# Kernel tuning notes

Measured on AMD Instinct MI355X. Metric: run time of the kernel, lower is better.

The kernel has to match this reference:

```python
import math
import jax
import jax.numpy as jnp
import numpy as np
from jax import lax

HEADS = 4
TOPK = 8


def _gelu(x):
    return jax.nn.gelu(x, approximate=False)


def _ln(x, g, b, eps=1e-5):
    m = x.mean(-1, keepdims=True)
    v = ((x - m) ** 2).mean(-1, keepdims=True)
    return (x - m) * lax.rsqrt(v + eps) * g + b


def setup_inputs() -> dict:
    key = jax.random.key(0)
    ks = jax.random.split(key, 16)
    B, T, N, C, A = 16, 16, 196, 768, 192

    def w(k, shape, s=0.02):
        return jax.random.normal(k, shape, jnp.float32) * s

    return dict(
        x=w(ks[0], (B, T, N + 1, C), 1.0),
        down_w=w(ks[1], (A, C)), down_b=jnp.zeros((A,), jnp.float32),
        ldw_w=w(ks[2], (A, 1, 3, 3), 0.1),
        lpw_w=w(ks[3], (A, A), 0.05),
        lnorm_g=jnp.ones((A,), jnp.float32), lnorm_b=jnp.zeros((A,), jnp.float32),
        tdw_w=w(ks[4], (A, 1, 3), 0.1),
        tpw_w=w(ks[5], (A, A), 0.05),
        tmlp_w1=w(ks[6], (2 * A, A), 0.05), tmlp_b1=jnp.zeros((2 * A,), jnp.float32),
        tmlp_w2=w(ks[7], (A, 2 * A), 0.05), tmlp_b2=jnp.zeros((A,), jnp.float32),
        tnorm_g=jnp.ones((A,), jnp.float32), tnorm_b=jnp.zeros((A,), jnp.float32),
        attn_in_w=w(ks[8], (3 * A, A), 0.05), attn_in_b=jnp.zeros((3 * A,), jnp.float32),
        attn_out_w=w(ks[9], (A, A), 0.05), attn_out_b=jnp.zeros((A,), jnp.float32),
        aproj_w=w(ks[10], (A, A), 0.05), aproj_b=jnp.zeros((A,), jnp.float32),
        anorm_g=jnp.ones((A,), jnp.float32), anorm_b=jnp.zeros((A,), jnp.float32),
        gate_w1=w(ks[11], (A, 2 * A), 0.05), gate_b1=jnp.zeros((A,), jnp.float32),
        gate_w2=w(ks[12], (3 * A, A), 0.05), gate_b2=jnp.zeros((3 * A,), jnp.float32),
        up_w=w(ks[13], (C, A), 0.02), up_b=jnp.zeros((C,), jnp.float32),
        cls_w=w(ks[14], (C, A), 0.02), cls_b=jnp.zeros((C,), jnp.float32),
    )


def reference(x, down_w, down_b, ldw_w, lpw_w, lnorm_g, lnorm_b, tdw_w, tpw_w,
              tmlp_w1, tmlp_b1, tmlp_w2, tmlp_b2, tnorm_g, tnorm_b,
              attn_in_w, attn_in_b, attn_out_w, attn_out_b, aproj_w, aproj_b,
              anorm_g, anorm_b, gate_w1, gate_b1, gate_w2, gate_b2,
              up_w, up_b, cls_w, cls_b):
    cls_tok = x[:, :, :1, :]
    patch = x[:, :, 1:, :]
    b, t, n, _ = patch.shape
    hw = int(math.isqrt(n))
    a = down_w.shape[0]

    # down projection: [b,t,n,C] -> [b,t,n,A]
    ph = jnp.einsum('btnc,ac->btna', patch, down_w) + down_b
    # temporal difference, delta[:,0]=0
    delta = jnp.concatenate([jnp.zeros_like(ph[:, :1]), ph[:, 1:] - ph[:, :-1]], axis=1)

    # --- local path: depthwise 3x3 -> GELU -> pointwise 1x1 -> LN ---
    loc = ph.reshape(b * t, hw, hw, a).transpose(0, 3, 1, 2)  # (bt) a h w
    loc = lax.conv_general_dilated(loc, ldw_w, (1, 1), 'SAME',
                                   feature_group_count=a,
                                   dimension_numbers=('NCHW', 'OIHW', 'NCHW'))
    loc = _gelu(loc)
    loc = jnp.einsum('bchw,dc->bdhw', loc, lpw_w)
    loc = loc.transpose(0, 2, 3, 1).reshape(b, t, n, a)
    local = _ln(loc, lnorm_g, lnorm_b)

    # --- transition path: depthwise temporal conv -> GELU -> pointwise -> MLP -> LN ---
    tr = delta.transpose(0, 2, 3, 1).reshape(b * n, a, t)  # (bn) a t
    tr = lax.conv_general_dilated(tr, tdw_w, (1,), 'SAME',
                                  feature_group_count=a,
                                  dimension_numbers=('NCH', 'OIH', 'NCH'))
    tr = _gelu(tr)
    tr = jnp.einsum('nct,dc->ndt', tr, tpw_w)
    tr = tr.reshape(b, n, a, t).transpose(0, 3, 1, 2)  # b t n a
    h1 = _gelu(jnp.einsum('btna,ha->btnh', tr, tmlp_w1) + tmlp_b1)
    tr = jnp.einsum('btnh,ah->btna', h1, tmlp_w2) + tmlp_b2
    transition = _ln(tr, tnorm_g, tnorm_b)

    # --- relation anchor path: topk gather -> temporal MHA -> scatter_add -> LN ---
    kk = min(TOPK, n)
    sal = jnp.abs(delta).mean(-1)  # b t n
    _, idx = lax.top_k(sal, kk)    # b t k
    bi = jnp.arange(b)[:, None, None]
    ti = jnp.arange(t)[None, :, None]
    anchor = (ph + delta)[bi, ti, idx]  # b t k a
    tok = anchor.transpose(0, 2, 1, 3).reshape(b * kk, t, a)  # (bk) t a
    qkv = tok @ attn_in_w.T + attn_in_b
    q, k_, v = jnp.split(qkv, 3, axis=-1)
    dh = a // HEADS

    def heads(z):
        return z.reshape(b * kk, t, HEADS, dh).transpose(0, 2, 1, 3)

    q, k_, v = heads(q), heads(k_), heads(v)
    att = jax.nn.softmax(jnp.einsum('bhqd,bhkd->bhqk', q, k_) / math.sqrt(dh), axis=-1)
    out = jnp.einsum('bhqk,bhkd->bhqd', att, v).transpose(0, 2, 1, 3).reshape(b * kk, t, a)
    out = out @ attn_out_w.T + attn_out_b
    out = out @ aproj_w.T + aproj_b
    anchor_tok = out.reshape(b, kk, t, a).transpose(0, 2, 1, 3)  # b t k a
    anchor_map = jnp.zeros_like(ph).at[bi, ti, idx].add(anchor_tok)
    anchor_map = _ln(anchor_map, anorm_g, anorm_b)

    # --- softmax-gated 3-way fusion ---
    dp = jnp.abs(delta).mean((1, 2))      # b a
    ap = anchor_tok.mean((1, 2))          # b a
    g = jnp.concatenate([dp, ap], axis=-1)
    g = _gelu(g @ gate_w1.T + gate_b1) @ gate_w2.T + gate_b2
    gw = jax.nn.softmax(g.reshape(b, 3, a), axis=1)[:, :, None, None, :]
    fused = gw[:, 0] * local + gw[:, 1] * transition + gw[:, 2] * anchor_map

    patch_out = patch + fused @ up_w.T + up_b
    cls_out = cls_tok + fused.mean(2, keepdims=True) @ cls_w.T + cls_b
    return jnp.concatenate([cls_out, patch_out], axis=2)
```

## Files before the change

### kernel.cpp

```cpp
#include <hip/hip_runtime.h>
#include <hip/hip_bf16.h>
#include <math.h>

constexpr int Bb  = 16;
constexpr int Tt  = 16;
constexpr int Nn  = 196;
constexpr int Cc  = 768;
constexpr int Aa  = 192;
constexpr int KK  = 8;
constexpr int NCAND = 16;
constexpr int BT  = Bb * Tt;
constexpr int BTN = BT * Nn;
constexpr int BKT = Bb * KK * Tt;
constexpr size_t SZ = (size_t)BTN * Aa;

typedef unsigned short ushortt;
typedef __attribute__((ext_vector_type(8))) short bf16x8;
typedef __attribute__((ext_vector_type(4))) float f32x4;
typedef __attribute__((ext_vector_type(4))) unsigned short u16x4;
typedef __attribute__((ext_vector_type(8))) unsigned short u16x8;

static __device__ __forceinline__ float gelu_f(float x) {
  return 0.5f * x * (1.0f + erff(x * 0.7071067811865476f));
}
static __device__ __forceinline__ ushortt f2bf(float f) {
  __hip_bfloat16 h = __float2bfloat16(f);
  return *reinterpret_cast<ushortt*>(&h);
}
static __device__ __forceinline__ float bf2f(ushortt u) {
  return __uint_as_float(((unsigned)u) << 16);
}
static __device__ __forceinline__ void gload16(const void* g, void* l) {
  __builtin_amdgcn_global_load_lds(
      (const __attribute__((address_space(1))) void*)g,
      (__attribute__((address_space(3))) void*)l, 16, 0, 0);
}

constexpr int S_down   = Aa * Cc;
constexpr int S_attnin = 3 * Aa * Aa;
constexpr int S_sq     = Aa * Aa;
constexpr int S_t      = 2 * Aa * Aa;
constexpr int O1 = S_down;
constexpr int O2 = O1 + S_attnin;
constexpr int O3 = O2 + S_sq;
constexpr int O4 = O3 + S_sq;
constexpr int O5 = O4 + S_sq;
constexpr int O6 = O5 + S_sq;
constexpr int O7 = O6 + S_t;
constexpr int O8 = O7 + S_t;
constexpr int OTOT = O8 + S_down;

__global__ void cvtw_kernel(const float* __restrict__ w0,
                            const float* __restrict__ w1,
                            const float* __restrict__ w2,
                            const float* __restrict__ w3,
                            const float* __restrict__ w4,
                            const float* __restrict__ w5,
                            const float* __restrict__ w6,
                            const float* __restrict__ w7,
                            const float* __restrict__ w8,
                            ushortt* __restrict__ outw) {
  int e = blockIdx.x * 256 + threadIdx.x;
  const float* src;
  int off;
  if (e < O1)      { src = w0; off = 0;  }
  else if (e < O2) { src = w1; off = O1; }
  else if (e < O3) { src = w2; off = O2; }
  else if (e < O4) { src = w3; off = O3; }
  else if (e < O5) { src = w4; off = O4; }
  else if (e < O6) { src = w5; off = O5; }
  else if (e < O7) { src = w6; off = O6; }
  else if (e < O8) { src = w7; off = O7; }
  else             { src = w8; off = O8; }
  outw[e] = f2bf(src[e - off]);
}

template <typename CT, int BIAS, int EPI>
__global__ __launch_bounds__(256) void gemm_lds(
    const ushortt* __restrict__ Ain, const ushortt* __restrict__ Wb,
    const float* __restrict__ bias, CT* __restrict__ Cout,
    const float* __restrict__ resid, int M, int Nc, int K) {
  __shared__ __align__(16) unsigned char smem[40960];
  ushortt (*As)[64 * 64] = (ushortt(*)[64 * 64])smem;
  ushortt (*Bs)[96 * 64] = (ushortt(*)[96 * 64])(smem + 2 * 64 * 64 * 2);
  const int tid = threadIdx.x;

  const int ncb = gridDim.x;
  const int nwg = ncb * gridDim.y;
  const int bid = blockIdx.y * ncb + blockIdx.x;
  const int cpx = nwg >> 3;
  const int swz = (bid & 7) * cpx + (bid >> 3);
  const int row0 = (swz / ncb) * 64;
  const int col0 = (swz % ncb) * 96;

  const int wid = tid >> 6;
  const int lane = tid & 63;
  const int wr = wid >> 1;
  const int wc = wid & 1;
  const int l15 = lane & 15;
  const int kgrp = lane >> 4;

  const int lr = lane >> 3;
  const int lc = 8 * ((lane & 7) ^ lr);

  f32x4 acc[2][3];
#pragma unroll
  for (int i = 0; i < 2; ++i)
#pragma unroll
    for (int j = 0; j < 3; ++j) acc[i][j] = (f32x4){0.f, 0.f, 0.f, 0.f};

#define ISSUE(buf, k0)                                                       \
  do {                                                                       \
    _Pragma("unroll") for (int i = 0; i < 2; ++i) {                          \
      int j = 2 * wid + i;                                                   \
      const ushortt* g =                                                     \
          Ain + (size_t)(row0 + 8 * j + lr) * K + (k0) + lc;                 \
      gload16(g, &As[buf][j * 512]);                                         \
    }                                                                        \
    _Pragma("unroll") for (int i = 0; i < 3; ++i) {                          \
      int j = 3 * wid + i;                                                   \
      const ushortt* g =                                                     \
          Wb + (size_t)(col0 + 8 * j + lr) * K + (k0) + lc;                  \
      gload16(g, &Bs[buf][j * 512]);                                         \
    }                                                                        \
  } while (0)

  ISSUE(0, 0);
  __syncthreads();

  const int nsteps = K >> 6;
  int cur = 0;
  for (int step = 0; step < nsteps; ++step) {
    const bool pref = (step + 1 < nsteps);
    if (pref) ISSUE(cur ^ 1, (step + 1) << 6);
#pragma unroll
    for (int kk = 0; kk < 2; ++kk) {
      const int cb = kk * 64 + kgrp * 16;
      bf16x8 af[2], bfv[3];
#pragma unroll
      for (int fm = 0; fm < 2; ++fm) {
        int r = wr * 32 + fm * 16 + l15;
        af[fm] = *(const bf16x8*)&As[cur][r * 64 +
                                          ((cb ^ ((r & 7) << 4)) >> 1)];
      }
#pragma unroll
      for (int fn = 0; fn < 3; ++fn) {
        int r = wc * 48 + fn * 16 + l15;
        bfv[fn] = *(const bf16x8*)&Bs[cur][r * 64 +
                                           ((cb ^ ((r & 7) << 4)) >> 1)];
      }
#pragma unroll
      for (int fm = 0; fm < 2; ++fm)
#pragma unroll
        for (int fn = 0; fn < 3; ++fn)
          acc[fm][fn] = __builtin_amdgcn_mfma_f32_16x16x32_bf16(
              af[fm], bfv[fn], acc[fm][fn], 0, 0, 0);
    }
    __syncthreads();
    cur ^= 1;
  }
#undef ISSUE

  constexpr int EP = 100;
  float* epi = (float*)smem;
#pragma unroll
  for (int fm = 0; fm < 2; ++fm) {
    int rl = wr * 32 + fm * 16 + kgrp * 4;
#pragma unroll
    for (int fn = 0; fn < 3; ++fn) {
      int cl = wc * 48 + fn * 16 + l15;
#pragma unroll
      for (int j = 0; j < 4; ++j)
        epi[(rl + j) * EP + cl] = acc[fm][fn][j];
    }
  }
  __syncthreads();
#pragma unroll
  for (int it = 0; it < 6; ++it) {
    int f = it * 256 + tid;
    int r = f / 24, c4 = f - r * 24;
    float4 v = *(const float4*)&epi[r * EP + c4 * 4];
    int c = col0 + c4 * 4;
    if (BIAS) {
      float4 bv = *(const float4*)(bias + c);
      v.x += bv.x; v.y += bv.y; v.z += bv.z; v.w += bv.w;
    }
    if (EPI == 1) {
      v.x = gelu_f(v.x); v.y = gelu_f(v.y);
      v.z = gelu_f(v.z); v.w = gelu_f(v.w);
    }
    int R = row0 + r;
    if constexpr (EPI == 2) {
      int bt2 = R / Nn, n2 = R - bt2 * Nn;
      size_t off = (size_t)(bt2 * (Nn + 1) + 1 + n2) * Nc + c;
      float4 rv = *(const float4*)(resid + off);
      v.x += rv.x; v.y += rv.y; v.z += rv.z; v.w += rv.w;
      *(float4*)((float*)Cout + off) = v;
    } else if constexpr (sizeof(CT) == 4) {
      *(float4*)((float*)Cout + (size_t)R * Nc + c) = v;
    } else {
      u16x4 ob = {f2bf(v.x), f2bf(v.y), f2bf(v.z), f2bf(v.w)};
      *(u16x4*)((ushortt*)Cout + (size_t)R * Nc + c) = ob;
    }
  }
}

template <int ROWMAP, typename CT, int BIAS, int EPI>
__global__ __launch_bounds__(256) void gemm_hyb(
    const float* __restrict__ Ain, const ushortt* __restrict__ Wb,
    const float* __restrict__ bias, CT* __restrict__ Cout,
    const float* __restrict__ resid, int M, int Nc, int K) {
  constexpr int PIT = 72;
  __shared__ __align__(16) unsigned char smem[43008];
  ushortt (*As)[64 * PIT] = (ushortt(*)[64 * PIT])smem;
  ushortt (*Bs)[96 * 64] = (ushortt(*)[96 * 64])(smem + 18432);
  const int tid = threadIdx.x;

  const int ncb = gridDim.x;
  const int nwg = ncb * gridDim.y;
  const int bid = blockIdx.y * ncb + blockIdx.x;
  const int cpx = nwg >> 3;
  const int swz = (bid & 7) * cpx + (bid >> 3);
  const int row0 = (swz / ncb) * 64;
  const int col0 = (swz % ncb) * 96;

  const int wid = tid >> 6;
  const int lane = tid & 63;
  const int wr = wid >> 1;
  const int wc = wid & 1;
  const int l15 = lane & 15;
  const int kgrp = lane >> 4;

  const int q16 = tid & 15;
  const int lr = lane >> 3;
  const int lc = 8 * ((lane & 7) ^ lr);

  const int nsteps = K >> 6;

  const float* arowf[4];
#pragma unroll
  for (int p = 0; p < 4; ++p) {
    int r = row0 + (tid >> 4) + 16 * p;
    if (ROWMAP) {
      int bt = r / Nn;
      int n = r - bt * Nn;
      arowf[p] = Ain + (size_t)(bt * (Nn + 1) + 1 + n) * K;
    } else {
      arowf[p] = Ain + (size_t)r * K;
    }
  }

  f32x4 acc[2][3];
#pragma unroll
  for (int i = 0; i < 2; ++i)
#pragma unroll
    for (int j = 0; j < 3; ++j) acc[i][j] = (f32x4){0.f, 0.f, 0.f, 0.f};

  float4 apre[4];

#define ISSUE_B(buf, k0)                                                     \
  do {                                                                       \
    _Pragma("unroll") for (int i = 0; i < 3; ++i) {                          \
      int j = 3 * wid + i;                                                   \
      const ushortt* g =                                                     \
          Wb + (size_t)(col0 + 8 * j + lr) * K + (k0) + lc;                  \
      gload16(g, &Bs[buf][j * 512]);                                         \
    }                                                                        \
  } while (0)

#define STAGE_LOAD_A(k0)                                                     \
  _Pragma("unroll") for (int p = 0; p < 4; ++p)                              \
      apre[p] = *(const float4*)(arowf[p] + (k0) + q16 * 4);

#define STAGE_WRITE_A(buf)                                                   \
  _Pragma("unroll") for (int p = 0; p < 4; ++p) {                            \
    u16x4 b = {f2bf(apre[p].x), f2bf(apre[p].y), f2bf(apre[p].z),            \
               f2bf(apre[p].w)};                                             \
    *(u16x4*)&As[buf][((tid >> 4) + 16 * p) * PIT + q16 * 4] = b;            \
  }

  ISSUE_B(0, 0);
  STAGE_LOAD_A(0);
  STAGE_WRITE_A(0);
  __syncthreads();

  int cur = 0;
  for (int step = 0; step < nsteps; ++step) {
    const bool pref = (step + 1 < nsteps);
    if (pref) {
      int k0 = (step + 1) << 6;
      ISSUE_B(cur ^ 1, k0);
      STAGE_LOAD_A(k0);
    }
#pragma unroll
    for (int kk = 0; kk < 2; ++kk) {
      const int cb = kk * 64 + kgrp * 16;
      bf16x8 af[2], bfv[3];
#pragma unroll
      for (int fm = 0; fm < 2; ++fm)
        af[fm] = *(const bf16x8*)&As[cur][(wr * 32 + fm * 16 + l15) * PIT +
                                          kk * 32 + kgrp * 8];
#pragma unroll
      for (int fn = 0; fn < 3; ++fn) {
        int r = wc * 48 + fn * 16 + l15;
        bfv[fn] = *(const bf16x8*)&Bs[cur][r * 64 +
                                           ((cb ^ ((r & 7) << 4)) >> 1)];
      }
#pragma unroll
      for (int fm = 0; fm < 2; ++fm)
#pragma unroll
        for (int fn = 0; fn < 3; ++fn)
          acc[fm][fn] = __builtin_amdgcn_mfma_f32_16x16x32_bf16(
              af[fm], bfv[fn], acc[fm][fn], 0, 0, 0);
    }
    if (pref) {
      STAGE_WRITE_A(cur ^ 1);
    }
    __syncthreads();
    cur ^= 1;
  }
#undef ISSUE_B
#undef STAGE_LOAD_A
#undef STAGE_WRITE_A

  constexpr int EP = 100;
  float* epi = (float*)smem;
#pragma unroll
  for (int fm = 0; fm < 2; ++fm) {
    int rl = wr * 32 + fm * 16 + kgrp * 4;
#pragma unroll
    for (int fn = 0; fn < 3; ++fn) {
      int cl = wc * 48 + fn * 16 + l15;
#pragma unroll
      for (int j = 0; j < 4; ++j)
        epi[(rl + j) * EP + cl] = acc[fm][fn][j];
    }
  }
  __syncthreads();
#pragma unroll
  for (int it = 0; it < 6; ++it) {
    int f = it * 256 + tid;
    int r = f / 24, c4 = f - r * 24;
    float4 v = *(const float4*)&epi[r * EP + c4 * 4];
    int c = col0 + c4 * 4;
    if (BIAS) {
      float4 bv = *(const float4*)(bias + c);
      v.x += bv.x; v.y += bv.y; v.z += bv.z; v.w += bv.w;
    }
    if (EPI == 1) {
      v.x = gelu_f(v.x); v.y = gelu_f(v.y);
      v.z = gelu_f(v.z); v.w = gelu_f(v.w);
    }
    int R = row0 + r;
    if constexpr (EPI == 2) {
      int bt2 = R / Nn, n2 = R - bt2 * Nn;
      size_t off = (size_t)(bt2 * (Nn + 1) + 1 + n2) * Nc + c;
      float4 rv = *(const float4*)(resid + off);
      v.x += rv.x; v.y += rv.y; v.z += rv.z; v.w += rv.w;
      *(float4*)((float*)Cout + off) = v;
    } else if constexpr (sizeof(CT) == 4) {
      *(float4*)((float*)Cout + (size_t)R * Nc + c) = v;
    } else {
      u16x4 ob = {f2bf(v.x), f2bf(v.y), f2bf(v.z), f2bf(v.w)};
      *(u16x4*)((ushortt*)Cout + (size_t)R * Nc + c) = ob;
    }
  }
}

__global__ void delta_kernel(const ushortt* __restrict__ ph,
                             ushortt* __restrict__ delta,
                             float* __restrict__ dppart) {
  int bt = blockIdx.x;
  int t = bt & 15;
  int a = threadIdx.x;
  const ushortt* cur = ph + (size_t)bt * Nn * Aa + a;
  ushortt* dl = delta + (size_t)bt * Nn * Aa + a;
  float acc = 0.f;
  if (t == 0) {
    for (int n = 0; n < Nn; ++n) dl[(size_t)n * Aa] = 0;
  } else {
    const ushortt* prev = cur - (size_t)Nn * Aa;
    for (int n = 0; n < Nn; ++n) {
      float d = bf2f(cur[(size_t)n * Aa]) - bf2f(prev[(size_t)n * Aa]);
      dl[(size_t)n * Aa] = f2bf(d);
      acc += fabsf(d);
    }
  }
  dppart[bt * Aa + a] = acc;
}

__global__ void sal_kernel(const ushortt* __restrict__ delta,
                           float* __restrict__ sal) {
  int row = blockIdx.x * 4 + (threadIdx.x >> 6);
  int lane = threadIdx.x & 63;
  const ushortt* d = delta + (size_t)row * Aa;
  float s = fabsf(bf2f(d[lane])) + fabsf(bf2f(d[lane + 64])) +
            fabsf(bf2f(d[lane + 128]));
#pragma unroll
  for (int off = 32; off > 0; off >>= 1) s += __shfl_xor(s, off, 64);
  if (lane == 0) sal[row] = s * (1.0f / 192.0f);
}

__global__ void topcand_kernel(const float* __restrict__ sal,
                               int* __restrict__ cand) {
  int bt = blockIdx.x;
  int lane = threadIdx.x;
  unsigned long long key[4];
#pragma unroll
  for (int j = 0; j < 4; ++j) {
    int n = lane + 64 * j;
    if (n < Nn) {
      unsigned fb = __float_as_uint(sal[(size_t)bt * Nn + n]);
      key[j] = ((unsigned long long)fb << 32) |
               (unsigned long long)(0xFFFFFFFFu - (unsigned)n);
    } else {
      key[j] = 0ULL;
    }
  }
  for (int r = 0; r < NCAND; ++r) {
    unsigned long long m = key[0];
    if (key[1] > m) m = key[1];
    if (key[2] > m) m = key[2];
    if (key[3] > m) m = key[3];
#pragma unroll
    for (int off = 32; off > 0; off >>= 1) {
      unsigned long long o = __shfl_xor(m, off, 64);
      if (o > m) m = o;
    }
    if (lane == 0)
      cand[bt * NCAND + r] = (int)(0xFFFFFFFFu - (unsigned)(m & 0xFFFFFFFFull));
#pragma unroll
    for (int j = 0; j < 4; ++j)
      if (key[j] == m) key[j] = 0ULL;
  }
}

__global__ void transpose_w(const float* __restrict__ w,
                            float* __restrict__ wT) {
  int e = blockIdx.x * 256 + threadIdx.x;
  int c = e / Aa, a = e - c * Aa;
  wT[e] = w[(size_t)a * Cc + c];
}

__global__ __launch_bounds__(192) void refine_kernel(
    const float* __restrict__ x, const float* __restrict__ wT,
    const int* __restrict__ cand, double* __restrict__ sal64) {
  int bt = blockIdx.x;
  int grp = blockIdx.y;
  int t = bt & 15;
  int a = threadIdx.x;
  if (t == 0) {
    if (a < 8) sal64[bt * NCAND + grp * 8 + a] = 0.0;
    return;
  }
  __shared__ double sdiff[8][Cc];
  const float* xt = x + ((size_t)bt * (Nn + 1) + 1) * Cc;
  const float* xp = xt - (size_t)(Nn + 1) * Cc;
  for (int g = 0; g < 8; ++g) {
    int n = cand[bt * NCAND + grp * 8 + g];
    const float* rt = xt + (size_t)n * Cc;
    const float* rp = xp + (size_t)n * Cc;
    for (int c = a; c < Cc; c += 192)
      sdiff[g][c] = (double)rt[c] - (double)rp[c];
  }
  __syncthreads();
  double acc[8] = {};
  for (int c = 0; c < Cc; ++c) {
    double wv = (double)wT[(size_t)c * Aa + a];
#pragma unroll
    for (int g = 0; g < 8; ++g) acc[g] = fma(wv, sdiff[g][c], acc[g]);
  }
  __shared__ double part[3][8];
  int wvx = a >> 6, ln = a & 63;
#pragma unroll
  for (int g = 0; g < 8; ++g) {
    double v = fabs(acc[g]);
#pragma unroll
    for (int off = 32; off > 0; off >>= 1) v += __shfl_xor(v, off, 64);
    if (ln == 0) part[wvx][g] = v;
  }
  __syncthreads();
  if (a < 8) {
    double s = part[0][a] + part[1][a] + part[2][a];
    sal64[bt * NCAND + grp * 8 + a] = s * (1.0 / 192.0);
  }
}

__global__ void select_kernel(const double* __restrict__ sal64,
                              const int* __restrict__ cand,
                              int* __restrict__ idx) {
  int bt = blockIdx.x;
  int t = bt & 15;
  int lane = threadIdx.x;
  if (t == 0) {
    if (lane < KK) idx[bt * KK + lane] = lane;
    return;
  }
  double v = (lane < NCAND) ? sal64[bt * NCAND + lane] : -1.0;
  int n = (lane < NCAND) ? cand[bt * NCAND + lane] : 0x7FFFFFFF;
  for (int r = 0; r < KK; ++r) {
    double bv = v;
    int bn = n, bl = lane;
#pragma unroll
    for (int off = 8; off >= 1; off >>= 1) {
      double ov = __shfl_xor(bv, off, 64);
      int on = __shfl_xor(bn, off, 64);
      int ol = __shfl_xor(bl, off, 64);
      if (ov > bv || (ov == bv && on < bn)) { bv = ov; bn = on; bl = ol; }
    }
    if (lane == 0) idx[bt * KK + r] = bn;
    if (lane == bl) v = -1.0;
  }
}

__global__ void gather_kernel(const ushortt* __restrict__ ph,
                              const ushortt* __restrict__ delta,
                              const int* __restrict__ idx,
                              ushortt* __restrict__ tok) {
  int row = blockIdx.x;
  int t = row & 15;
  int bk = row >> 4;
  int b = bk >> 3, k = bk & 7;
  int a = threadIdx.x;
  int n = idx[(b * 16 + t) * KK + k];
  size_t off = ((size_t)(b * 16 + t) * Nn + n) * Aa + a;
  tok[(size_t)row * Aa + a] = f2bf(bf2f(ph[off]) + bf2f(delta[off]));
}

__global__ __launch_bounds__(256) void attn_core(
    const float* __restrict__ qkv, float* __restrict__ o) {
  constexpr int P = 580;
  __shared__ float sq[16 * P];
  __shared__ float ssc[4][16][17];
  int bk = blockIdx.x;
  int tid = threadIdx.x;
  const float* src = qkv + (size_t)bk * 16 * 576;
  for (int e = tid; e < 16 * 144; e += 256) {
    int r = e / 144, c4 = e % 144;
    float4 v = *(const float4*)(src + r * 576 + c4 * 4);
    *(float4*)(&sq[r * P + c4 * 4]) = v;
  }
  __syncthreads();
  int h = tid >> 6, lane = tid & 63;
#pragma unroll
  for (int s4 = 0; s4 < 4; ++s4) {
    int e = lane + 64 * s4;
    int i = e >> 4, j = e & 15;
    const float* q = sq + i * P + h * 48;
    const float* k2 = sq + j * P + 192 + h * 48;
    float s = 0.f;
#pragma unroll
    for (int d = 0; d < 48; ++d) s = fmaf(q[d], k2[d], s);
    ssc[h][i][j] = s * 0.14433756729740643f;
  }
  __syncthreads();
  if (lane < 16) {
    float* r = ssc[h][lane];
    float mx = r[0];
    for (int j = 1; j < 16; ++j) mx = fmaxf(mx, r[j]);
    float sum = 0.f;
    for (int j = 0; j < 16; ++j) {
      float ev = expf(r[j] - mx);
      r[j] = ev;
      sum += ev;
    }
    float inv = 1.0f / sum;
    for (int j = 0; j < 16; ++j) r[j] *= inv;
  }
  __syncthreads();
#pragma unroll
  for (int s4 = 0; s4 < 12; ++s4) {
    int e = lane + 64 * s4;
    int i = e / 48, d = e - i * 48;
    float s = 0.f;
#pragma unroll
    for (int j = 0; j < 16; ++j)
      s = fmaf(ssc[h][i][j], sq[j * P + 384 + h * 48 + d], s);
    o[((size_t)bk * 16 + i) * 192 + h * 48 + d] = s;
  }
}

__global__ void appart_kernel(const float* __restrict__ attout,
                              float* __restrict__ appart) {
  int bk = blockIdx.x;
  int a = threadIdx.x;
  float s = 0.f;
  for (int t = 0; t < Tt; ++t)
    s += attout[((size_t)bk * Tt + t) * Aa + a];
  appart[bk * Aa + a] = s;
}

__global__ void ln32_kernel(float* __restrict__ buf,
                            const float* __restrict__ g,
                            const float* __restrict__ bb) {
  size_t row = (size_t)blockIdx.x * 4 + (threadIdx.x >> 6);
  int lane = threadIdx.x & 63;
  float* p = buf + row * Aa;
  float v0 = p[lane], v1 = p[lane + 64], v2 = p[lane + 128];
  float s = v0 + v1 + v2;
#pragma unroll
  for (int off = 32; off > 0; off >>= 1) s += __shfl_xor(s, off, 64);
  float m = s * (1.0f / 192.0f);
  float d0 = v0 - m, d1 = v1 - m, d2 = v2 - m;
  float ss = d0 * d0 + d1 * d1 + d2 * d2;
#pragma unroll
  for (int off = 32; off > 0; off >>= 1) ss += __shfl_xor(ss, off, 64);
  float inv = rsqrtf(ss * (1.0f / 192.0f) + 1e-5f);
  p[lane] = d0 * inv * g[lane] + bb[lane];
  p[lane + 64] = d1 * inv * g[lane + 64] + bb[lane + 64];
  p[lane + 128] = d2 * inv * g[lane + 128] + bb[lane + 128];
}

__global__ void conv2d_kernel(const ushortt* __restrict__ ph,
                              const float* __restrict__ ldw,
                              ushortt* __restrict__ og) {
  size_t e = (size_t)blockIdx.x * 256 + threadIdx.x;
  int a = (int)(e % Aa);
  size_t r = e / Aa;
  int n = (int)(r % Nn);
  int bt = (int)(r / Nn);
  int y = n / 14, x = n % 14;
  const ushortt* base = ph + (size_t)bt * Nn * Aa + a;
  const float* w = ldw + a * 9;
  float s = 0.f;
#pragma unroll
  for (int dy = -1; dy <= 1; ++dy) {
    int yy = y + dy;
    if (yy < 0 || yy >= 14) continue;
#pragma unroll
    for (int dx = -1; dx <= 1; ++dx) {
      int xc = x + dx;
      if (xc < 0 || xc >= 14) continue;
      s = fmaf(bf2f(base[(size_t)(yy * 14 + xc) * Aa]),
               w[(dy + 1) * 3 + (dx + 1)], s);
    }
  }
  og[e] = f2bf(gelu_f(s));
}

__global__ void conv1d_kernel(const ushortt* __restrict__ delta,
                              const float* __restrict__ tdw,
                              ushortt* __restrict__ og) {
  size_t e = (size_t)blockIdx.x * 256 + threadIdx.x;
  int a = (int)(e % Aa);
  size_t r = e / Aa;
  int n = (int)(r % Nn);
  int bt = (int)(r / Nn);
  int t = bt & 15, b = bt >> 4;
  const float* w = tdw + a * 3;
  float s = 0.f;
#pragma unroll
  for (int j = 0; j < 3; ++j) {
    int tt = t + j - 1;
    if (tt >= 0 && tt < Tt)
      s = fmaf(bf2f(delta[((size_t)(b * Tt + tt) * Nn + n) * Aa + a]), w[j], s);
  }
  og[e] = f2bf(gelu_f(s));
}

__global__ void ln_kernel(ushortt* __restrict__ buf,
                          const float* __restrict__ g,
                          const float* __restrict__ bb) {
  size_t row = (size_t)blockIdx.x * 4 + (threadIdx.x >> 6);
  int lane = threadIdx.x & 63;
  ushortt* p = buf + row * Aa;
  float v0 = bf2f(p[lane]), v1 = bf2f(p[lane + 64]), v2 = bf2f(p[lane + 128]);
  float s = v0 + v1 + v2;
#pragma unroll
  for (int off = 32; off > 0; off >>= 1) s += __shfl_xor(s, off, 64);
  float m = s * (1.0f / 192.0f);
  float d0 = v0 - m, d1 = v1 - m, d2 = v2 - m;
  float ss = d0 * d0 + d1 * d1 + d2 * d2;
#pragma unroll
  for (int off = 32; off > 0; off >>= 1) ss += __shfl_xor(ss, off, 64);
  float inv = rsqrtf(ss * (1.0f / 192.0f) + 1e-5f);
  p[lane] = f2bf(d0 * inv * g[lane] + bb[lane]);
  p[lane + 64] = f2bf(d1 * inv * g[lane + 64] + bb[lane + 64]);
  p[lane + 128] = f2bf(d2 * inv * g[lane + 128] + bb[lane + 128]);
}

__global__ void scatter_pos(const int* __restrict__ idx,
                            short* __restrict__ posmap) {
  int bt = blockIdx.x;
  int k = threadIdx.x;
  if (k < KK) posmap[bt * Nn + idx[bt * KK + k]] = (short)(k + 1);
}

__global__ void gate_kernel(const float* __restrict__ dppart,
                            const float* __restrict__ appart,
                            const float* __restrict__ w1,
                            const float* __restrict__ b1,
                            const float* __restrict__ w2,
                            const float* __restrict__ b2,
                            float* __restrict__ gw) {
  int b = blockIdx.x;
  __shared__ float sg[2 * Aa];
  __shared__ float sh[Aa];
  int tid = threadIdx.x;
  {
    float d = 0.f;
    for (int t2 = 0; t2 < Tt; ++t2) d += dppart[(b * Tt + t2) * Aa + tid];
    sg[tid] = d * (1.0f / 3136.0f);
    float a = 0.f;
    for (int k2 = 0; k2 < KK; ++k2) a += appart[(b * KK + k2) * Aa + tid];
    sg[Aa + tid] = a * (1.0f / 128.0f);
  }
  __syncthreads();
  {
    const float* w = w1 + (size_t)tid * 2 * Aa;
    float s = b1[tid];
#pragma unroll 8
    for (int j = 0; j < 2 * Aa; ++j) s = fmaf(sg[j], w[j], s);
    sh[tid] = gelu_f(s);
  }
  __syncthreads();
  float v[3];
#pragma unroll
  for (int i = 0; i < 3; ++i) {
    const float* w = w2 + (size_t)(i * Aa + tid) * Aa;
    float s = b2[i * Aa + tid];
#pragma unroll 8
    for (int j = 0; j < Aa; ++j) s = fmaf(sh[j], w[j], s);
    v[i] = s;
  }
  float mx = fmaxf(v[0], fmaxf(v[1], v[2]));
  float e0 = expf(v[0] - mx), e1 = expf(v[1] - mx), e2 = expf(v[2] - mx);
  float inv = 1.0f / (e0 + e1 + e2);
  gw[(b * 3 + 0) * Aa + tid] = e0 * inv;
  gw[(b * 3 + 1) * Aa + tid] = e1 * inv;
  gw[(b * 3 + 2) * Aa + tid] = e2 * inv;
}

__global__ void fused_kernel(const ushortt* __restrict__ local,
                             const ushortt* __restrict__ trans,
                             const float* __restrict__ attln,
                             const short* __restrict__ posmap,
                             const float* __restrict__ anb,
                             const float* __restrict__ gw,
                             ushortt* __restrict__ fused,
                             float* __restrict__ fmean) {
  int bt = blockIdx.x;
  int b = bt >> 4, t = bt & 15;
  int a = threadIdx.x;
  float g0 = gw[(b * 3 + 0) * Aa + a];
  float g1 = gw[(b * 3 + 1) * Aa + a];
  float g2 = gw[(b * 3 + 2) * Aa + a];
  float ab = anb[a];
  size_t base = (size_t)bt * Nn * Aa + a;
  float acc = 0.f;
  for (int n = 0; n < Nn; ++n) {
    size_t o = base + (size_t)n * Aa;
    short pos = posmap[bt * Nn + n];
    float am = pos ? attln[(((size_t)(b * KK + pos - 1) * Tt) + t) * Aa + a]
                   : ab;
    float f = g0 * bf2f(local[o]) + g1 * bf2f(trans[o]) + g2 * am;
    fused[o] = f2bf(f);
    acc += f;
  }
  fmean[bt * Aa + a] = acc;
}

__global__ void cls_kernel(const float* __restrict__ fmean,
                           const float* __restrict__ cw,
                           const float* __restrict__ cb,
                           const float* __restrict__ x,
                           float* __restrict__ out) {
  int bt = blockIdx.x;
  __shared__ float fm[Aa];
  int tid = threadIdx.x;
  if (tid < Aa) fm[tid] = fmean[bt * Aa + tid] * (1.0f / 196.0f);
  __syncthreads();
  for (int c = tid; c < Cc; c += 256) {
    const float* w = cw + (size_t)c * Aa;
    float s = cb[c];
#pragma unroll 8
    for (int a = 0; a < Aa; ++a) s = fmaf(fm[a], w[a], s);
    size_t off = (size_t)bt * (Nn + 1) * Cc + c;
    out[off] = x[off] + s;
  }
}

extern "C" void kernel_launch(void* const* d_in, const int* in_sizes, int n_in,
                              void* d_out, int out_size, void* d_ws,
                              size_t ws_size, hipStream_t stream) {
  const float* x = (const float*)d_in[0];
  const float* down_w = (const float*)d_in[1];
  const float* down_b = (const float*)d_in[2];
  const float* ldw_w = (const float*)d_in[3];
  const float* lpw_w = (const float*)d_in[4];
  const float* lnorm_g = (const float*)d_in[5];
  const float* lnorm_b = (const float*)d_in[6];
  const float* tdw_w = (const float*)d_in[7];
  const float* tpw_w = (const float*)d_in[8];
  const float* tmlp_w1 = (const float*)d_in[9];
  const float* tmlp_b1 = (const float*)d_in[10];
  const float* tmlp_w2 = (const float*)d_in[11];
  const float* tmlp_b2 = (const float*)d_in[12];
  const float* tnorm_g = (const float*)d_in[13];
  const float* tnorm_b = (const float*)d_in[14];
  const float* attn_in_w = (const float*)d_in[15];
  const float* attn_in_b = (const float*)d_in[16];
  const float* attn_out_w = (const float*)d_in[17];
  const float* attn_out_b = (const float*)d_in[18];
  const float* aproj_w = (const float*)d_in[19];
  const float* aproj_b = (const float*)d_in[20];
  const float* anorm_g = (const float*)d_in[21];
  const float* anorm_b = (const float*)d_in[22];
  const float* gate_w1 = (const float*)d_in[23];
  const float* gate_b1 = (const float*)d_in[24];
  const float* gate_w2 = (const float*)d_in[25];
  const float* gate_b2 = (const float*)d_in[26];
  const float* up_w = (const float*)d_in[27];
  const float* up_b = (const float*)d_in[28];
  const float* cls_w = (const float*)d_in[29];
  const float* cls_b = (const float*)d_in[30];
  float* out = (float*)d_out;

  float* ws = (float*)d_ws;
  float* W0 = ws;
  float* W1 = W0 + SZ;
  float* W2 = W1 + SZ;
  float* W3 = W2 + 2 * SZ;
  float* sal = W3 + SZ;
  float* attout = sal + BTN;
  float* dppart = attout + (size_t)BKT * Aa;
  float* appart = dppart + (size_t)BT * Aa;
  float* gw = appart + (size_t)Bb * KK * Aa;
  float* fmean = gw + (size_t)Bb * 3 * Aa;
  double* sal64 = (double*)(fmean + (size_t)BT * Aa);
  int* cand = (int*)(sal64 + (size_t)BT * NCAND);
  int* idx = cand + (size_t)BT * NCAND;
  float* wT = (float*)(idx + (size_t)BT * KK);
  short* posmap = (short*)(wT + (size_t)Cc * Aa);
  ushortt* wbuf = (ushortt*)(posmap + (size_t)BT * Nn);

  ushortt* wb_down   = wbuf;
  ushortt* wb_attnin = wbuf + O1;
  ushortt* wb_attnout= wbuf + O2;
  ushortt* wb_aproj  = wbuf + O3;
  ushortt* wb_lpw    = wbuf + O4;
  ushortt* wb_tpw    = wbuf + O5;
  ushortt* wb_t1     = wbuf + O6;
  ushortt* wb_t2     = wbuf + O7;
  ushortt* wb_up     = wbuf + O8;

  ushortt* ph_b    = (ushortt*)W0;
  ushortt* trp_b   = (ushortt*)W0;
  ushortt* delta_b = (ushortt*)W1;
  ushortt* trans_b = (ushortt*)W1;
  ushortt* locg_b  = (ushortt*)W2;
  ushortt* trg_b   = (ushortt*)W2;
  ushortt* h1_b    = (ushortt*)W2;
  ushortt* fused_b = (ushortt*)W2;
  ushortt* local_b = (ushortt*)W3;

  ushortt* tok_b = (ushortt*)W2;
  float* qkvb  = W2 + (size_t)BKT * Aa / 2;
  float* obuf  = qkvb + (size_t)BKT * 3 * Aa;
  float* proj1 = obuf + (size_t)BKT * Aa;

  cvtw_kernel<<<OTOT / 256, 256, 0, stream>>>(
      down_w, attn_in_w, attn_out_w, aproj_w, lpw_w, tpw_w, tmlp_w1,
      tmlp_w2, up_w, wbuf);
  transpose_w<<<(Cc * Aa) / 256, 256, 0, stream>>>(down_w, wT);
  gemm_hyb<1, ushortt, 1, 0><<<dim3(2, 784), 256, 0, stream>>>(
      x, wb_down, down_b, ph_b, nullptr, BTN, Aa, Cc);
  delta_kernel<<<BT, Aa, 0, stream>>>(ph_b, delta_b, dppart);
  sal_kernel<<<BTN / 4, 256, 0, stream>>>(delta_b, sal);
  topcand_kernel<<<BT, 64, 0, stream>>>(sal, cand);
  refine_kernel<<<dim3(BT, 2), 192, 0, stream>>>(x, wT, cand, sal64);
  select_kernel<<<BT, 64, 0, stream>>>(sal64, cand, idx);
  gather_kernel<<<BKT, Aa, 0, stream>>>(ph_b, delta_b, idx, tok_b);
  gemm_lds<float, 1, 0><<<dim3(6, 32), 256, 0, stream>>>(
      tok_b, wb_attnin, attn_in_b, qkvb, nullptr, BKT, 3 * Aa, Aa);
  attn_core<<<Bb * KK, 256, 0, stream>>>(qkvb, obuf);
  gemm_hyb<0, float, 1, 0><<<dim3(2, 32), 256, 0, stream>>>(
      obuf, wb_attnout, attn_out_b, proj1, nullptr, BKT, Aa, Aa);
  gemm_hyb<0, float, 1, 0><<<dim3(2, 32), 256, 0, stream>>>(
      proj1, wb_aproj, aproj_b, attout, nullptr, BKT, Aa, Aa);
  appart_kernel<<<Bb * KK, Aa, 0, stream>>>(attout, appart);
  ln32_kernel<<<BKT / 4, 256, 0, stream>>>(attout, anorm_g, anorm_b);
  hipMemsetAsync(posmap, 0, (size_t)BT * Nn * sizeof(short), stream);
  scatter_pos<<<BT, 64, 0, stream>>>(idx, posmap);
  conv2d_kernel<<<(unsigned)(SZ / 256), 256, 0, stream>>>(ph_b, ldw_w, locg_b);
  gemm_lds<ushortt, 0, 0><<<dim3(2, 784), 256, 0, stream>>>(
      locg_b, wb_lpw, nullptr, local_b, nullptr, BTN, Aa, Aa);
  ln_kernel<<<BTN / 4, 256, 0, stream>>>(local_b, lnorm_g, lnorm_b);
  conv1d_kernel<<<(unsigned)(SZ / 256), 256, 0, stream>>>(delta_b, tdw_w, trg_b);
  gemm_lds<ushortt, 0, 0><<<dim3(2, 784), 256, 0, stream>>>(
      trg_b, wb_tpw, nullptr, trp_b, nullptr, BTN, Aa, Aa);
  gemm_lds<ushortt, 1, 1><<<dim3(4, 784), 256, 0, stream>>>(
      trp_b, wb_t1, tmlp_b1, h1_b, nullptr, BTN, 2 * Aa, Aa);
  gemm_lds<ushortt, 1, 0><<<dim3(2, 784), 256, 0, stream>>>(
      h1_b, wb_t2, tmlp_b2, trans_b, nullptr, BTN, Aa, 2 * Aa);
  ln_kernel<<<BTN / 4, 256, 0, stream>>>(trans_b, tnorm_g, tnorm_b);
  gate_kernel<<<Bb, Aa, 0, stream>>>(dppart, appart, gate_w1, gate_b1,
                                     gate_w2, gate_b2, gw);
  fused_kernel<<<BT, Aa, 0, stream>>>(local_b, trans_b, attout, posmap,
                                      anorm_b, gw, fused_b, fmean);
  gemm_lds<float, 1, 2><<<dim3(8, 784), 256, 0, stream>>>(
      fused_b, wb_up, up_b, out, x, BTN, Cc, Aa);
  cls_kernel<<<BT, 256, 0, stream>>>(fmean, cls_w, cls_b, x, out);
}
```

Measured before the change: 576.3 us.

## Split delta and fused kernels into 14-row chunks and fold saliency into delta

The delta and fused elementwise kernels previously ran one block per (b,t) with a serial loop over 196 rows, only 256 blocks in total. They now launch 14 blocks per (b,t), each covering 14 rows, and write per-chunk partial sums that the gate and cls kernels reduce. The separate saliency kernel is merged into the delta kernel via wave shuffles and a small shared-memory reduction, which saves one pass over delta. The cost is extra partial-sum buffers and slightly more reduction work in the consumers; the kernel also keeps a leftover empty loop.

```diff
diff --git a/kernel.cpp b/kernel.cpp
--- a/kernel.cpp
+++ b/kernel.cpp
@@ -9,6 +9,7 @@
 constexpr int Aa  = 192;
 constexpr int KK  = 8;
 constexpr int NCAND = 16;
+constexpr int NCH = 14;
 constexpr int BT  = Bb * Tt;
 constexpr int BTN = BT * Nn;
 constexpr int BKT = Bb * KK * Tt;
@@ -367,38 +368,43 @@
   }
 }
 
-__global__ void delta_kernel(const ushortt* __restrict__ ph,
-                             ushortt* __restrict__ delta,
-                             float* __restrict__ dppart) {
-  int bt = blockIdx.x;
+__global__ __launch_bounds__(192) void delta14_kernel(
+    const ushortt* __restrict__ ph, ushortt* __restrict__ delta,
+    float* __restrict__ dppart2, float* __restrict__ sal) {
+  int blk = blockIdx.x;
+  int bt = blk / NCH, chunk = blk - bt * NCH;
   int t = bt & 15;
   int a = threadIdx.x;
-  const ushortt* cur = ph + (size_t)bt * Nn * Aa + a;
-  ushortt* dl = delta + (size_t)bt * Nn * Aa + a;
+  int n0 = chunk * 14;
+  __shared__ float spart[3][14];
+  const ushortt* cur = ph + ((size_t)bt * Nn + n0) * Aa + a;
+  ushortt* dl = delta + ((size_t)bt * Nn + n0) * Aa + a;
+  int wv = a >> 6, ln = a & 63;
   float acc = 0.f;
   if (t == 0) {
-    for (int n = 0; n < Nn; ++n) dl[(size_t)n * Aa] = 0;
-  } else {
-    const ushortt* prev = cur - (size_t)Nn * Aa;
-    for (int n = 0; n < Nn; ++n) {
-      float d = bf2f(cur[(size_t)n * Aa]) - bf2f(prev[(size_t)n * Aa]);
-      dl[(size_t)n * Aa] = f2bf(d);
-      acc += fabsf(d);
-    }
-  }
-  dppart[bt * Aa + a] = acc;
-}
-
-__global__ void sal_kernel(const ushortt* __restrict__ delta,
-                           float* __restrict__ sal) {
-  int row = blockIdx.x * 4 + (threadIdx.x >> 6);
-  int lane = threadIdx.x & 63;
-  const ushortt* d = delta + (size_t)row * Aa;
-  float s = fabsf(bf2f(d[lane])) + fabsf(bf2f(d[lane + 64])) +
-            fabsf(bf2f(d[lane + 128]));
-#pragma unroll
-  for (int off = 32; off > 0; off >>= 1) s += __shfl_xor(s, off, 64);
-  if (lane == 0) sal[row] = s * (1.0f / 192.0f);
+    for (int i = 0; i < 14; ++i) dl[(size_t)i * Aa] = 0;
+    if (a < 14) sal[(size_t)bt * Nn + n0 + a] = 0.f;
+    if (a == 0)
+      for (int q = 0; q < Aa; ++q) ;
+    dppart2[(size_t)blk * Aa + a] = 0.f;
+    return;
+  }
+  const ushortt* prev = cur - (size_t)Nn * Aa;
+  for (int i = 0; i < 14; ++i) {
+    float d = bf2f(cur[(size_t)i * Aa]) - bf2f(prev[(size_t)i * Aa]);
+    dl[(size_t)i * Aa] = f2bf(d);
+    float ad = fabsf(d);
+    acc += ad;
+    float s = ad;
+#pragma unroll
+    for (int off = 32; off > 0; off >>= 1) s += __shfl_xor(s, off, 64);
+    if (ln == 0) spart[wv][i] = s;
+  }
+  dppart2[(size_t)blk * Aa + a] = acc;
+  __syncthreads();
+  if (a < 14)
+    sal[(size_t)bt * Nn + n0 + a] =
+        (spart[0][a] + spart[1][a] + spart[2][a]) * (1.0f / 192.0f);
 }
 
 __global__ void topcand_kernel(const float* __restrict__ sal,
@@ -686,7 +692,7 @@
   if (k < KK) posmap[bt * Nn + idx[bt * KK + k]] = (short)(k + 1);
 }
 
-__global__ void gate_kernel(const float* __restrict__ dppart,
+__global__ void gate_kernel(const float* __restrict__ dppart2,
                             const float* __restrict__ appart,
                             const float* __restrict__ w1,
                             const float* __restrict__ b1,
@@ -699,7 +705,8 @@
   int tid = threadIdx.x;
   {
     float d = 0.f;
-    for (int t2 = 0; t2 < Tt; ++t2) d += dppart[(b * Tt + t2) * Aa + tid];
+    for (int t2 = 0; t2 < Tt * NCH; ++t2)
+      d += dppart2[(size_t)(b * Tt * NCH + t2) * Aa + tid];
     sg[tid] = d * (1.0f / 3136.0f);
     float a = 0.f;
     for (int k2 = 0; k2 < KK; ++k2) a += appart[(b * KK + k2) * Aa + tid];
@@ -731,36 +738,35 @@
   gw[(b * 3 + 2) * Aa + tid] = e2 * inv;
 }
 
-__global__ void fused_kernel(const ushortt* __restrict__ local,
-                             const ushortt* __restrict__ trans,
-                             const float* __restrict__ attln,
-                             const short* __restrict__ posmap,
-                             const float* __restrict__ anb,
-                             const float* __restrict__ gw,
-                             ushortt* __restrict__ fused,
-                             float* __restrict__ fmean) {
-  int bt = blockIdx.x;
+__global__ __launch_bounds__(192) void fused14_kernel(
+    const ushortt* __restrict__ local, const ushortt* __restrict__ trans,
+    const float* __restrict__ attln, const short* __restrict__ posmap,
+    const float* __restrict__ anb, const float* __restrict__ gw,
+    ushortt* __restrict__ fused, float* __restrict__ fpart) {
+  int blk = blockIdx.x;
+  int bt = blk / NCH, chunk = blk - bt * NCH;
   int b = bt >> 4, t = bt & 15;
   int a = threadIdx.x;
+  int n0 = chunk * 14;
   float g0 = gw[(b * 3 + 0) * Aa + a];
   float g1 = gw[(b * 3 + 1) * Aa + a];
   float g2 = gw[(b * 3 + 2) * Aa + a];
   float ab = anb[a];
-  size_t base = (size_t)bt * Nn * Aa + a;
+  size_t base = ((size_t)bt * Nn + n0) * Aa + a;
   float acc = 0.f;
-  for (int n = 0; n < Nn; ++n) {
-    size_t o = base + (size_t)n * Aa;
-    short pos = posmap[bt * Nn + n];
+  for (int i = 0; i < 14; ++i) {
+    size_t o = base + (size_t)i * Aa;
+    short pos = posmap[bt * Nn + n0 + i];
     float am = pos ? attln[(((size_t)(b * KK + pos - 1) * Tt) + t) * Aa + a]
                    : ab;
     float f = g0 * bf2f(local[o]) + g1 * bf2f(trans[o]) + g2 * am;
     fused[o] = f2bf(f);
     acc += f;
   }
-  fmean[bt * Aa + a] = acc;
-}
-
-__global__ void cls_kernel(const float* __restrict__ fmean,
+  fpart[(size_t)blk * Aa + a] = acc;
+}
+
+__global__ void cls_kernel(const float* __restrict__ fpart,
                            const float* __restrict__ cw,
                            const float* __restrict__ cb,
                            const float* __restrict__ x,
@@ -768,7 +774,12 @@
   int bt = blockIdx.x;
   __shared__ float fm[Aa];
   int tid = threadIdx.x;
-  if (tid < Aa) fm[tid] = fmean[bt * Aa + tid] * (1.0f / 196.0f);
+  if (tid < Aa) {
+    float s = 0.f;
+    for (int ch = 0; ch < NCH; ++ch)
+      s += fpart[(size_t)(bt * NCH + ch) * Aa + tid];
+    fm[tid] = s * (1.0f / 196.0f);
+  }
   __syncthreads();
   for (int c = tid; c < Cc; c += 256) {
     const float* w = cw + (size_t)c * Aa;
@@ -823,11 +834,11 @@
   float* W3 = W2 + 2 * SZ;
   float* sal = W3 + SZ;
   float* attout = sal + BTN;
-  float* dppart = attout + (size_t)BKT * Aa;
-  float* appart = dppart + (size_t)BT * Aa;
+  float* dppart2 = attout + (size_t)BKT * Aa;
+  float* appart = dppart2 + (size_t)BT * NCH * Aa;
   float* gw = appart + (size_t)Bb * KK * Aa;
-  float* fmean = gw + (size_t)Bb * 3 * Aa;
-  double* sal64 = (double*)(fmean + (size_t)BT * Aa);
+  float* fpart = gw + (size_t)Bb * 3 * Aa;
+  double* sal64 = (double*)(fpart + (size_t)BT * NCH * Aa);
   int* cand = (int*)(sal64 + (size_t)BT * NCAND);
   int* idx = cand + (size_t)BT * NCAND;
   float* wT = (float*)(idx + (size_t)BT * KK);
@@ -865,8 +876,7 @@
   transpose_w<<<(Cc * Aa) / 256, 256, 0, stream>>>(down_w, wT);
   gemm_hyb<1, ushortt, 1, 0><<<dim3(2, 784), 256, 0, stream>>>(
       x, wb_down, down_b, ph_b, nullptr, BTN, Aa, Cc);
-  delta_kernel<<<BT, Aa, 0, stream>>>(ph_b, delta_b, dppart);
-  sal_kernel<<<BTN / 4, 256, 0, stream>>>(delta_b, sal);
+  delta14_kernel<<<BT * NCH, 192, 0, stream>>>(ph_b, delta_b, dppart2, sal);
   topcand_kernel<<<BT, 64, 0, stream>>>(sal, cand);
   refine_kernel<<<dim3(BT, 2), 192, 0, stream>>>(x, wT, cand, sal64);
   select_kernel<<<BT, 64, 0, stream>>>(sal64, cand, idx);
@@ -894,11 +904,12 @@
   gemm_lds<ushortt, 1, 0><<<dim3(2, 784), 256, 0, stream>>>(
       h1_b, wb_t2, tmlp_b2, trans_b, nullptr, BTN, Aa, 2 * Aa);
   ln_kernel<<<BTN / 4, 256, 0, stream>>>(trans_b, tnorm_g, tnorm_b);
-  gate_kernel<<<Bb, Aa, 0, stream>>>(dppart, appart, gate_w1, gate_b1,
+  gate_kernel<<<Bb, Aa, 0, stream>>>(dppart2, appart, gate_w1, gate_b1,
                                      gate_w2, gate_b2, gw);
-  fused_kernel<<<BT, Aa, 0, stream>>>(local_b, trans_b, attout, posmap,
-                                      anorm_b, gw, fused_b, fmean);
+  fused14_kernel<<<BT * NCH, 192, 0, stream>>>(local_b, trans_b, attout,
+                                               posmap, anorm_b, gw, fused_b,
+                                               fpart);
   gemm_lds<float, 1, 2><<<dim3(8, 784), 256, 0, stream>>>(
       fused_b, wb_up, up_b, out, x, BTN, Cc, Aa);
-  cls_kernel<<<BT, 256, 0, stream>>>(fmean, cls_w, cls_b, x, out);
-}
+  cls_kernel<<<BT, 256, 0, stream>>>(fpart, cls_w, cls_b, x, out);
+}
```

Result: faster. 524.8 us (-8.9%).
